# Performance work log

Hardware: AMD Instinct MI355X
Metric: run time of the kernel (lower is better)

Reference implementation:

```python
import jax, jax.numpy as jnp
import numpy as np

N, K, DIM = 50000, 16, 256
SLOPE = 0.2

def _leaky(x):
    return jnp.where(x >= 0, x, SLOPE * x)

def _mlp(x, w, b):
    # torch nn.Linear followed by LeakyReLU(0.2); w is [in, out]
    return _leaky(x @ w + b)

def setup_inputs() -> dict:
    key = jax.random.key(0)
    ks = jax.random.split(key, 14)
    d4, d2 = DIM // 4, DIM // 2
    def lin(k, i, o):
        kw, kb = jax.random.split(k)
        s = 1.0 / np.sqrt(i)
        return (jax.random.uniform(kw, (i, o), jnp.float32, -s, s),
                jax.random.uniform(kb, (o,), jnp.float32, -s, s))
    w_res, b_res = lin(ks[0], DIM, DIM)
    w_init, b_init = lin(ks[1], DIM, d4)
    w_g1, b_g1 = lin(ks[2], 4, d4)
    w_g2, b_g2 = lin(ks[3], 4, d2)
    w_fin, b_fin = lin(ks[4], DIM, DIM)
    return {
        "input_features": jax.random.normal(ks[5], (N, DIM), jnp.float32),
        "geom_features": jax.random.normal(ks[6], (N, K, 4), jnp.float32),
        "closest_indices": jax.random.randint(ks[7], (N, K), 0, N, jnp.int32),
        "w_res": w_res, "b_res": b_res,
        "w_init": w_init, "b_init": b_init,
        "w_g1": w_g1, "b_g1": b_g1,
        "w_g2": w_g2, "b_g2": b_g2,
        "w_fin": w_fin, "b_fin": b_fin,
    }

def _lfa(feat, geom, idx, w_g, b_g):
    # feat: [N, d]; geom: [N, K, 4]; idx: [N, K]
    g = _mlp(geom, w_g, b_g)                 # [N, K, d]
    gathered = feat[idx]                      # [N, K, d] gather over points
    combined = jnp.concatenate([g, gathered], axis=-1)  # [N, K, 2d]
    return jnp.mean(combined, axis=1)         # [N, 2d]

def reference(input_features, geom_features, closest_indices,
              w_res, b_res, w_init, b_init, w_g1, b_g1, w_g2, b_g2,
              w_fin, b_fin):
    residual = _mlp(input_features, w_res, b_res)            # [N, DIM]
    a = _mlp(input_features, w_init, b_init)                 # [N, DIM/4]
    a = _lfa(a, geom_features, closest_indices, w_g1, b_g1)  # [N, DIM/2]
    a = _lfa(a, geom_features, closest_indices, w_g2, b_g2)  # [N, DIM]
    a = _mlp(a, w_fin, b_fin)                                # [N, DIM]
    return a + residual
```

## Files before the change

### kernel.cpp

```cpp
#include <hip/hip_runtime.h>

#define DIM 256
#define KNN 16
#define SLOPE 0.2f

typedef unsigned short u16;
typedef __attribute__((ext_vector_type(8))) unsigned short u16x8;
typedef __attribute__((ext_vector_type(4))) unsigned short u16x4;
typedef __attribute__((ext_vector_type(8))) short s16x8;
typedef __attribute__((ext_vector_type(4))) float f32x4;

__device__ __forceinline__ float leaky(float x) { return x >= 0.f ? x : SLOPE * x; }
__device__ __forceinline__ u16 f2bu(float f) {
    unsigned int u = __float_as_uint(f);
    u = (u + 0x7FFFu + ((u >> 16) & 1u)) >> 16;
    return (u16)u;
}
__device__ __forceinline__ float bu2f(u16 h) {
    return __uint_as_float(((unsigned int)h) << 16);
}

__global__ __launch_bounds__(256) void k_prep(
    const float* __restrict__ w_res, const float* __restrict__ w_init,
    const float* __restrict__ w_fin, u16* __restrict__ wT1, u16* __restrict__ wT3)
{
    const int c = blockIdx.x, t = threadIdx.x;
    if (c < 256)      wT1[c * 256 + t] = f2bu(w_res[t * 256 + c]);
    else if (c < 320) wT1[c * 256 + t] = f2bu(w_init[t * 64 + (c - 256)]);
    else              wT3[(c - 320) * 256 + t] = f2bu(w_fin[t * 256 + (c - 320)]);
}

#define APAD 264
#define BPAD 40
__global__ __launch_bounds__(256) void k_gemm1(
    const float* __restrict__ in, const u16* __restrict__ wT1,
    const float* __restrict__ b_res, const float* __restrict__ b_init,
    float* __restrict__ resid, u16* __restrict__ a1, int N)
{
    __shared__ u16 A_s[64 * APAD];
    __shared__ u16 B_s[320 * BPAD];
    const int t = threadIdx.x;
    const int base = blockIdx.x * 64;

    {
        const int row = t >> 2, seg = t & 3;
        const int grow = min(base + row, N - 1);
        const float* src = in + (size_t)grow * DIM + seg * 64;
        u16* dst = &A_s[row * APAD + seg * 64];
        #pragma unroll
        for (int j = 0; j < 8; ++j) {
            float4 f0 = *(const float4*)(src + j * 8);
            float4 f1 = *(const float4*)(src + j * 8 + 4);
            u16x8 p;
            p[0] = f2bu(f0.x); p[1] = f2bu(f0.y); p[2] = f2bu(f0.z); p[3] = f2bu(f0.w);
            p[4] = f2bu(f1.x); p[5] = f2bu(f1.y); p[6] = f2bu(f1.z); p[7] = f2bu(f1.w);
            *(u16x8*)(dst + j * 8) = p;
        }
    }

    f32x4 acc[4][5];
    #pragma unroll
    for (int i = 0; i < 4; ++i)
        #pragma unroll
        for (int j = 0; j < 5; ++j)
            acc[i][j] = (f32x4){0.f, 0.f, 0.f, 0.f};

    const int w = t >> 6, lane = t & 63;
    const int llow = lane & 15, lhi = lane >> 4;

    for (int ks = 0; ks < 8; ++ks) {
        u16x8 breg[5];
        #pragma unroll
        for (int j = 0; j < 5; ++j) {
            int id = t + 256 * j;
            int col = id >> 2, kg = id & 3;
            breg[j] = *(const u16x8*)(wT1 + col * 256 + ks * 32 + kg * 8);
        }
        __syncthreads();
        #pragma unroll
        for (int j = 0; j < 5; ++j) {
            int id = t + 256 * j;
            int col = id >> 2, kg = id & 3;
            *(u16x8*)(&B_s[col * BPAD + kg * 8]) = breg[j];
        }
        __syncthreads();

        s16x8 afrag[4];
        #pragma unroll
        for (int rt = 0; rt < 4; ++rt)
            afrag[rt] = *(const s16x8*)(&A_s[(rt * 16 + llow) * APAD + ks * 32 + lhi * 8]);
        #pragma unroll
        for (int ci = 0; ci < 5; ++ci) {
            const int ct = w * 5 + ci;
            s16x8 bfrag = *(const s16x8*)(&B_s[(ct * 16 + llow) * BPAD + lhi * 8]);
            #pragma unroll
            for (int rt = 0; rt < 4; ++rt)
                acc[rt][ci] = __builtin_amdgcn_mfma_f32_16x16x32_bf16(
                    afrag[rt], bfrag, acc[rt][ci], 0, 0, 0);
        }
    }

    #pragma unroll
    for (int ci = 0; ci < 5; ++ci) {
        const int ct = w * 5 + ci;
        const int col = ct * 16 + llow;
        if (col < 256) {
            const float bias = b_res[col];
            #pragma unroll
            for (int rt = 0; rt < 4; ++rt)
                #pragma unroll
                for (int r = 0; r < 4; ++r) {
                    int row = base + rt * 16 + lhi * 4 + r;
                    if (row < N)
                        resid[(size_t)row * DIM + col] = leaky(acc[rt][ci][r] + bias);
                }
        } else {
            const int c2 = col - 256;
            const float bias = b_init[c2];
            #pragma unroll
            for (int rt = 0; rt < 4; ++rt)
                #pragma unroll
                for (int r = 0; r < 4; ++r) {
                    int row = base + rt * 16 + lhi * 4 + r;
                    if (row < N)
                        a1[(size_t)row * 64 + c2] = f2bu(leaky(acc[rt][ci][r] + bias));
                }
        }
    }
}

__global__ __launch_bounds__(256) void k_lfa1(
    const float* __restrict__ geom, const int* __restrict__ idx,
    const float* __restrict__ w_g1, const float* __restrict__ b_g1,
    const u16* __restrict__ a1, u16* __restrict__ a2, int N)
{
    __shared__ float geom_s[16 * KNN * 4];
    __shared__ int idx_s[16 * KNN];
    const int t = threadIdx.x;
    const int base = blockIdx.x * 16;

    {
        size_t off = (size_t)base * 64 + t * 4;
        size_t mx = (size_t)N * 64 - 4;
        if (off > mx) off = mx;
        *(float4*)&geom_s[t * 4] = *(const float4*)(geom + off);
        int io = base * KNN + t;
        if (t < 256) idx_s[t] = idx[min(io, N * KNN - 1)];
    }
    __syncthreads();

    const int pt = t >> 4, s = t & 15;
    const int n = base + pt;

    float wr[4][4], bb[4];
    #pragma unroll
    for (int r = 0; r < 4; ++r)
        #pragma unroll
        for (int j = 0; j < 4; ++j)
            wr[r][j] = w_g1[r * 64 + s * 4 + j];
    #pragma unroll
    for (int j = 0; j < 4; ++j) bb[j] = b_g1[s * 4 + j];

    float accM[4] = {0.f, 0.f, 0.f, 0.f};
    const float4* g4 = (const float4*)&geom_s[pt * 64];
    #pragma unroll
    for (int k = 0; k < KNN; ++k) {
        float4 g = g4[k];
        #pragma unroll
        for (int j = 0; j < 4; ++j)
            accM[j] += leaky(g.x * wr[0][j] + g.y * wr[1][j] + g.z * wr[2][j] + g.w * wr[3][j] + bb[j]);
    }

    float accG[4] = {0.f, 0.f, 0.f, 0.f};
    #pragma unroll
    for (int k = 0; k < KNN; ++k) {
        u16x4 u = *(const u16x4*)(a1 + (size_t)idx_s[pt * KNN + k] * 64 + s * 4);
        #pragma unroll
        for (int j = 0; j < 4; ++j) accG[j] += bu2f(u[j]);
    }

    if (n < N) {
        u16x4 pm, pg;
        #pragma unroll
        for (int j = 0; j < 4; ++j) {
            pm[j] = f2bu(accM[j] * 0.0625f);
            pg[j] = f2bu(accG[j] * 0.0625f);
        }
        *(u16x4*)(a2 + (size_t)n * 128 + s * 4) = pm;
        *(u16x4*)(a2 + (size_t)n * 128 + 64 + s * 4) = pg;
    }
}

__global__ __launch_bounds__(256) void k_lfa2_fin(
    const float* __restrict__ geom, const int* __restrict__ idx,
    const float* __restrict__ w_g2, const float* __restrict__ b_g2,
    const u16* __restrict__ a2, const u16* __restrict__ wT3,
    const float* __restrict__ b_fin, float* __restrict__ out, int N)
{
    __shared__ u16 a3_s[64 * APAD];
    __shared__ u16 B_s[256 * BPAD];
    __shared__ float geom_s[64 * KNN * 4];
    __shared__ int idx_s[64 * KNN];
    const int t = threadIdx.x;
    const int base = blockIdx.x * 64;

    {
        size_t mx = (size_t)N * 64 - 4;
        #pragma unroll
        for (int j = 0; j < 4; ++j) {
            size_t off = (size_t)base * 64 + t * 4 + j * 1024;
            if (off > mx) off = mx;
            *(float4*)&geom_s[t * 4 + j * 1024] = *(const float4*)(geom + off);
        }
        int imx = N * KNN - 1;
        #pragma unroll
        for (int j = 0; j < 4; ++j) {
            int off = base * KNN + t + j * 256;
            idx_s[t + j * 256] = idx[min(off, imx)];
        }
    }
    __syncthreads();

    {
        const int c = t & 127, h = t >> 7;
        const float w0 = w_g2[c], w1 = w_g2[128 + c], w2 = w_g2[256 + c],
                    w3 = w_g2[384 + c], bb = b_g2[c];
        for (int p = 0; p < 32; ++p) {
            const int pt = h * 32 + p;
            float acc = 0.f;
            const float4* g4 = (const float4*)&geom_s[pt * 64];
            #pragma unroll
            for (int k = 0; k < KNN; ++k) {
                float4 g = g4[k];
                acc += leaky(g.x * w0 + g.y * w1 + g.z * w2 + g.w * w3 + bb);
            }
            a3_s[pt * APAD + c] = f2bu(acc * 0.0625f);
        }
    }
    {
        const int pt = t >> 2, q = t & 3;
        float acc[32];
        #pragma unroll
        for (int j = 0; j < 32; ++j) acc[j] = 0.f;
        for (int k = 0; k < KNN; ++k) {
            const u16* row = a2 + (size_t)idx_s[pt * KNN + k] * 128 + q * 32;
            #pragma unroll
            for (int v = 0; v < 4; ++v) {
                u16x8 u = *(const u16x8*)(row + v * 8);
                #pragma unroll
                for (int j = 0; j < 8; ++j) acc[v * 8 + j] += bu2f(u[j]);
            }
        }
        #pragma unroll
        for (int v = 0; v < 4; ++v) {
            u16x8 p;
            #pragma unroll
            for (int j = 0; j < 8; ++j) p[j] = f2bu(acc[v * 8 + j] * 0.0625f);
            *(u16x8*)(&a3_s[pt * APAD + 128 + q * 32 + v * 8]) = p;
        }
    }

    f32x4 acc[4][4];
    #pragma unroll
    for (int i = 0; i < 4; ++i)
        #pragma unroll
        for (int j = 0; j < 4; ++j)
            acc[i][j] = (f32x4){0.f, 0.f, 0.f, 0.f};

    const int w = t >> 6, lane = t & 63;
    const int llow = lane & 15, lhi = lane >> 4;

    for (int ks = 0; ks < 8; ++ks) {
        u16x8 breg[4];
        #pragma unroll
        for (int kg = 0; kg < 4; ++kg)
            breg[kg] = *(const u16x8*)(wT3 + t * 256 + ks * 32 + kg * 8);
        __syncthreads();
        #pragma unroll
        for (int kg = 0; kg < 4; ++kg)
            *(u16x8*)(&B_s[t * BPAD + kg * 8]) = breg[kg];
        __syncthreads();

        s16x8 afrag[4];
        #pragma unroll
        for (int rt = 0; rt < 4; ++rt)
            afrag[rt] = *(const s16x8*)(&a3_s[(rt * 16 + llow) * APAD + ks * 32 + lhi * 8]);
        #pragma unroll
        for (int ci = 0; ci < 4; ++ci) {
            const int ct = w * 4 + ci;
            s16x8 bfrag = *(const s16x8*)(&B_s[(ct * 16 + llow) * BPAD + lhi * 8]);
            #pragma unroll
            for (int rt = 0; rt < 4; ++rt)
                acc[rt][ci] = __builtin_amdgcn_mfma_f32_16x16x32_bf16(
                    afrag[rt], bfrag, acc[rt][ci], 0, 0, 0);
        }
    }

    #pragma unroll
    for (int ci = 0; ci < 4; ++ci) {
        const int ct = w * 4 + ci;
        const int col = ct * 16 + llow;
        const float bias = b_fin[col];
        #pragma unroll
        for (int rt = 0; rt < 4; ++rt)
            #pragma unroll
            for (int r = 0; r < 4; ++r) {
                int row = base + rt * 16 + lhi * 4 + r;
                if (row < N) {
                    size_t o = (size_t)row * DIM + col;
                    out[o] = leaky(acc[rt][ci][r] + bias) + out[o];
                }
            }
    }
}

extern "C" void kernel_launch(void* const* d_in, const int* in_sizes, int n_in,
                              void* d_out, int out_size, void* d_ws, size_t ws_size,
                              hipStream_t stream) {
    const float* in    = (const float*)d_in[0];
    const float* geom  = (const float*)d_in[1];
    const int*   idx   = (const int*)d_in[2];
    const float* w_res = (const float*)d_in[3];
    const float* b_res = (const float*)d_in[4];
    const float* w_init= (const float*)d_in[5];
    const float* b_init= (const float*)d_in[6];
    const float* w_g1  = (const float*)d_in[7];
    const float* b_g1  = (const float*)d_in[8];
    const float* w_g2  = (const float*)d_in[9];
    const float* b_g2  = (const float*)d_in[10];
    const float* w_fin = (const float*)d_in[11];
    const float* b_fin = (const float*)d_in[12];
    float* out = (float*)d_out;

    const int N = in_sizes[0] / DIM;

    char* ws = (char*)d_ws;
    u16* a1  = (u16*)ws;
    u16* a2  = (u16*)(ws + (size_t)N * 64 * 2);
    u16* wT1 = (u16*)(ws + (size_t)N * (64 + 128) * 2);
    u16* wT3 = wT1 + 320 * 256;

    k_prep<<<576, 256, 0, stream>>>(w_res, w_init, w_fin, wT1, wT3);
    k_gemm1<<<(N + 63) / 64, 256, 0, stream>>>(in, wT1, b_res, b_init, out, a1, N);
    k_lfa1<<<(N + 15) / 16, 256, 0, stream>>>(geom, idx, w_g1, b_g1, a1, a2, N);
    k_lfa2_fin<<<(N + 63) / 64, 256, 0, stream>>>(geom, idx, w_g2, b_g2, a2, wT3, b_fin, out, N);
}
```

Before: 292.7 us.

## Read GEMM weight fragments directly from global memory, drop LDS staging

Both GEMM kernels now load the B (weight) MFMA fragments straight from global/L2 instead of staging them in shared memory, which removes two barriers per k-step. The fused lfa2 kernel also reads geom and idx directly from global instead of copying them into LDS first. Together these cut LDS usage so more blocks fit per CU, with a launch-bounds hint of 3 blocks, and add unroll pragmas. The cost is that every wave re-reads the weights from cache, and loads are less coalesced, so performance now depends on L2/L1 bandwidth.

```diff
diff --git a/kernel.cpp b/kernel.cpp
--- a/kernel.cpp
+++ b/kernel.cpp
@@ -31,14 +31,12 @@
 }
 
 #define APAD 264
-#define BPAD 40
-__global__ __launch_bounds__(256) void k_gemm1(
+__global__ __launch_bounds__(256, 3) void k_gemm1(
     const float* __restrict__ in, const u16* __restrict__ wT1,
     const float* __restrict__ b_res, const float* __restrict__ b_init,
     float* __restrict__ resid, u16* __restrict__ a1, int N)
 {
     __shared__ u16 A_s[64 * APAD];
-    __shared__ u16 B_s[320 * BPAD];
     const int t = threadIdx.x;
     const int base = blockIdx.x * 64;
 
@@ -57,6 +55,7 @@
             *(u16x8*)(dst + j * 8) = p;
         }
     }
+    __syncthreads();
 
     f32x4 acc[4][5];
     #pragma unroll
@@ -68,23 +67,8 @@
     const int w = t >> 6, lane = t & 63;
     const int llow = lane & 15, lhi = lane >> 4;
 
+    #pragma unroll
     for (int ks = 0; ks < 8; ++ks) {
-        u16x8 breg[5];
-        #pragma unroll
-        for (int j = 0; j < 5; ++j) {
-            int id = t + 256 * j;
-            int col = id >> 2, kg = id & 3;
-            breg[j] = *(const u16x8*)(wT1 + col * 256 + ks * 32 + kg * 8);
-        }
-        __syncthreads();
-        #pragma unroll
-        for (int j = 0; j < 5; ++j) {
-            int id = t + 256 * j;
-            int col = id >> 2, kg = id & 3;
-            *(u16x8*)(&B_s[col * BPAD + kg * 8]) = breg[j];
-        }
-        __syncthreads();
-
         s16x8 afrag[4];
         #pragma unroll
         for (int rt = 0; rt < 4; ++rt)
@@ -92,7 +76,7 @@
         #pragma unroll
         for (int ci = 0; ci < 5; ++ci) {
             const int ct = w * 5 + ci;
-            s16x8 bfrag = *(const s16x8*)(&B_s[(ct * 16 + llow) * BPAD + lhi * 8]);
+            s16x8 bfrag = *(const s16x8*)(wT1 + (size_t)(ct * 16 + llow) * 256 + ks * 32 + lhi * 8);
             #pragma unroll
             for (int rt = 0; rt < 4; ++rt)
                 acc[rt][ci] = __builtin_amdgcn_mfma_f32_16x16x32_bf16(
@@ -145,7 +129,7 @@
         if (off > mx) off = mx;
         *(float4*)&geom_s[t * 4] = *(const float4*)(geom + off);
         int io = base * KNN + t;
-        if (t < 256) idx_s[t] = idx[min(io, N * KNN - 1)];
+        idx_s[t] = idx[min(io, N * KNN - 1)];
     }
     __syncthreads();
 
@@ -191,44 +175,26 @@
     }
 }
 
-__global__ __launch_bounds__(256) void k_lfa2_fin(
+__global__ __launch_bounds__(256, 3) void k_lfa2_fin(
     const float* __restrict__ geom, const int* __restrict__ idx,
     const float* __restrict__ w_g2, const float* __restrict__ b_g2,
     const u16* __restrict__ a2, const u16* __restrict__ wT3,
     const float* __restrict__ b_fin, float* __restrict__ out, int N)
 {
     __shared__ u16 a3_s[64 * APAD];
-    __shared__ u16 B_s[256 * BPAD];
-    __shared__ float geom_s[64 * KNN * 4];
-    __shared__ int idx_s[64 * KNN];
     const int t = threadIdx.x;
     const int base = blockIdx.x * 64;
-
-    {
-        size_t mx = (size_t)N * 64 - 4;
-        #pragma unroll
-        for (int j = 0; j < 4; ++j) {
-            size_t off = (size_t)base * 64 + t * 4 + j * 1024;
-            if (off > mx) off = mx;
-            *(float4*)&geom_s[t * 4 + j * 1024] = *(const float4*)(geom + off);
-        }
-        int imx = N * KNN - 1;
-        #pragma unroll
-        for (int j = 0; j < 4; ++j) {
-            int off = base * KNN + t + j * 256;
-            idx_s[t + j * 256] = idx[min(off, imx)];
-        }
-    }
-    __syncthreads();
 
     {
         const int c = t & 127, h = t >> 7;
         const float w0 = w_g2[c], w1 = w_g2[128 + c], w2 = w_g2[256 + c],
                     w3 = w_g2[384 + c], bb = b_g2[c];
+        #pragma unroll 4
         for (int p = 0; p < 32; ++p) {
             const int pt = h * 32 + p;
+            const int grow = min(base + pt, N - 1);
+            const float4* g4 = (const float4*)(geom + (size_t)grow * 64);
             float acc = 0.f;
-            const float4* g4 = (const float4*)&geom_s[pt * 64];
             #pragma unroll
             for (int k = 0; k < KNN; ++k) {
                 float4 g = g4[k];
@@ -239,11 +205,14 @@
     }
     {
         const int pt = t >> 2, q = t & 3;
+        const int irow = min(base + pt, N - 1);
         float acc[32];
         #pragma unroll
         for (int j = 0; j < 32; ++j) acc[j] = 0.f;
+        #pragma unroll 4
         for (int k = 0; k < KNN; ++k) {
-            const u16* row = a2 + (size_t)idx_s[pt * KNN + k] * 128 + q * 32;
+            const int id = idx[(size_t)irow * KNN + k];
+            const u16* row = a2 + (size_t)id * 128 + q * 32;
             #pragma unroll
             for (int v = 0; v < 4; ++v) {
                 u16x8 u = *(const u16x8*)(row + v * 8);
@@ -259,6 +228,7 @@
             *(u16x8*)(&a3_s[pt * APAD + 128 + q * 32 + v * 8]) = p;
         }
     }
+    __syncthreads();
 
     f32x4 acc[4][4];
     #pragma unroll
@@ -270,17 +240,8 @@
     const int w = t >> 6, lane = t & 63;
     const int llow = lane & 15, lhi = lane >> 4;
 
+    #pragma unroll
     for (int ks = 0; ks < 8; ++ks) {
-        u16x8 breg[4];
-        #pragma unroll
-        for (int kg = 0; kg < 4; ++kg)
-            breg[kg] = *(const u16x8*)(wT3 + t * 256 + ks * 32 + kg * 8);
-        __syncthreads();
-        #pragma unroll
-        for (int kg = 0; kg < 4; ++kg)
-            *(u16x8*)(&B_s[t * BPAD + kg * 8]) = breg[kg];
-        __syncthreads();
-
         s16x8 afrag[4];
         #pragma unroll
         for (int rt = 0; rt < 4; ++rt)
@@ -288,7 +249,7 @@
         #pragma unroll
         for (int ci = 0; ci < 4; ++ci) {
             const int ct = w * 4 + ci;
-            s16x8 bfrag = *(const s16x8*)(&B_s[(ct * 16 + llow) * BPAD + lhi * 8]);
+            s16x8 bfrag = *(const s16x8*)(wT3 + (size_t)(ct * 16 + llow) * 256 + ks * 32 + lhi * 8);
             #pragma unroll
             for (int rt = 0; rt < 4; ++rt)
                 acc[rt][ci] = __builtin_amdgcn_mfma_f32_16x16x32_bf16(
```

Result: slower. 358.4 us (+22.4%).

## Split LFA2 gather into separate high-occupancy kernel before final GEMM

Applied to the files above, without the earlier changes.

The fused lfa2+final-GEMM kernel is split in two. A standalone gather kernel averages neighbour rows of a2 into a half-width buffer a3h, using 16 points per block and all 16 loads issued before any accumulation. The GEMM kernel then loads a3h rows directly into shared memory. lfa1's gather is also batched so all loads are in flight together. This aims to expose more memory-level parallelism for the random gathers, at the cost of an extra launch and a round trip of a3h through global memory. a3h aliases the a1 region, which is assumed dead by then.

```diff
diff --git a/kernel.cpp b/kernel.cpp
--- a/kernel.cpp
+++ b/kernel.cpp
@@ -144,8 +144,7 @@
         size_t mx = (size_t)N * 64 - 4;
         if (off > mx) off = mx;
         *(float4*)&geom_s[t * 4] = *(const float4*)(geom + off);
-        int io = base * KNN + t;
-        if (t < 256) idx_s[t] = idx[min(io, N * KNN - 1)];
+        idx_s[t] = idx[min(base * KNN + t, N * KNN - 1)];
     }
     __syncthreads();
 
@@ -172,12 +171,14 @@
     }
 
     float accG[4] = {0.f, 0.f, 0.f, 0.f};
-    #pragma unroll
-    for (int k = 0; k < KNN; ++k) {
-        u16x4 u = *(const u16x4*)(a1 + (size_t)idx_s[pt * KNN + k] * 64 + s * 4);
-        #pragma unroll
-        for (int j = 0; j < 4; ++j) accG[j] += bu2f(u[j]);
-    }
+    u16x4 v[KNN];
+    #pragma unroll
+    for (int k = 0; k < KNN; ++k)
+        v[k] = *(const u16x4*)(a1 + (size_t)idx_s[pt * KNN + k] * 64 + s * 4);
+    #pragma unroll
+    for (int k = 0; k < KNN; ++k)
+        #pragma unroll
+        for (int j = 0; j < 4; ++j) accG[j] += bu2f(v[k][j]);
 
     if (n < N) {
         u16x4 pm, pg;
@@ -191,16 +192,45 @@
     }
 }
 
-__global__ __launch_bounds__(256) void k_lfa2_fin(
-    const float* __restrict__ geom, const int* __restrict__ idx,
-    const float* __restrict__ w_g2, const float* __restrict__ b_g2,
-    const u16* __restrict__ a2, const u16* __restrict__ wT3,
-    const float* __restrict__ b_fin, float* __restrict__ out, int N)
-{
-    __shared__ u16 a3_s[64 * APAD];
+__global__ __launch_bounds__(256) void k_gather3(
+    const int* __restrict__ idx, const u16* __restrict__ a2,
+    u16* __restrict__ a3h, int N)
+{
+    __shared__ int idx_s[16 * KNN];
+    const int t = threadIdx.x;
+    const int base = blockIdx.x * 16;
+    idx_s[t] = idx[min(base * KNN + t, N * KNN - 1)];
+    __syncthreads();
+
+    const int pt = t >> 4, s = t & 15;
+    const int n = base + pt;
+
+    u16x8 v[KNN];
+    #pragma unroll
+    for (int k = 0; k < KNN; ++k)
+        v[k] = *(const u16x8*)(a2 + (size_t)idx_s[pt * KNN + k] * 128 + s * 8);
+
+    float acc[8] = {0.f, 0.f, 0.f, 0.f, 0.f, 0.f, 0.f, 0.f};
+    #pragma unroll
+    for (int k = 0; k < KNN; ++k)
+        #pragma unroll
+        for (int j = 0; j < 8; ++j) acc[j] += bu2f(v[k][j]);
+
+    u16x8 p;
+    #pragma unroll
+    for (int j = 0; j < 8; ++j) p[j] = f2bu(acc[j] * 0.0625f);
+    if (n < N) *(u16x8*)(a3h + (size_t)n * 128 + s * 8) = p;
+}
+
+__global__ __launch_bounds__(256) void k_gemm3(
+    const float* __restrict__ geom, const float* __restrict__ w_g2,
+    const float* __restrict__ b_g2, const u16* __restrict__ a3h,
+    const u16* __restrict__ wT3, const float* __restrict__ b_fin,
+    float* __restrict__ out, int N)
+{
+    __shared__ u16 A_s[64 * APAD];
     __shared__ u16 B_s[256 * BPAD];
-    __shared__ float geom_s[64 * KNN * 4];
-    __shared__ int idx_s[64 * KNN];
+    __shared__ float geom_s[64 * 64];
     const int t = threadIdx.x;
     const int base = blockIdx.x * 64;
 
@@ -212,12 +242,13 @@
             if (off > mx) off = mx;
             *(float4*)&geom_s[t * 4 + j * 1024] = *(const float4*)(geom + off);
         }
-        int imx = N * KNN - 1;
-        #pragma unroll
-        for (int j = 0; j < 4; ++j) {
-            int off = base * KNN + t + j * 256;
-            idx_s[t + j * 256] = idx[min(off, imx)];
-        }
+        const int row = t >> 2, q = t & 3;
+        const int grow = min(base + row, N - 1);
+        const u16* src = a3h + (size_t)grow * 128 + q * 32;
+        u16* dst = &A_s[row * APAD + 128 + q * 32];
+        #pragma unroll
+        for (int j = 0; j < 4; ++j)
+            *(u16x8*)(dst + j * 8) = *(const u16x8*)(src + j * 8);
     }
     __syncthreads();
 
@@ -225,38 +256,17 @@
         const int c = t & 127, h = t >> 7;
         const float w0 = w_g2[c], w1 = w_g2[128 + c], w2 = w_g2[256 + c],
                     w3 = w_g2[384 + c], bb = b_g2[c];
+        #pragma unroll 4
         for (int p = 0; p < 32; ++p) {
             const int pt = h * 32 + p;
+            const float4* g4 = (const float4*)&geom_s[pt * 64];
             float acc = 0.f;
-            const float4* g4 = (const float4*)&geom_s[pt * 64];
             #pragma unroll
             for (int k = 0; k < KNN; ++k) {
                 float4 g = g4[k];
                 acc += leaky(g.x * w0 + g.y * w1 + g.z * w2 + g.w * w3 + bb);
             }
-            a3_s[pt * APAD + c] = f2bu(acc * 0.0625f);
-        }
-    }
-    {
-        const int pt = t >> 2, q = t & 3;
-        float acc[32];
-        #pragma unroll
-        for (int j = 0; j < 32; ++j) acc[j] = 0.f;
-        for (int k = 0; k < KNN; ++k) {
-            const u16* row = a2 + (size_t)idx_s[pt * KNN + k] * 128 + q * 32;
-            #pragma unroll
-            for (int v = 0; v < 4; ++v) {
-                u16x8 u = *(const u16x8*)(row + v * 8);
-                #pragma unroll
-                for (int j = 0; j < 8; ++j) acc[v * 8 + j] += bu2f(u[j]);
-            }
-        }
-        #pragma unroll
-        for (int v = 0; v < 4; ++v) {
-            u16x8 p;
-            #pragma unroll
-            for (int j = 0; j < 8; ++j) p[j] = f2bu(acc[v * 8 + j] * 0.0625f);
-            *(u16x8*)(&a3_s[pt * APAD + 128 + q * 32 + v * 8]) = p;
+            A_s[pt * APAD + c] = f2bu(acc * 0.0625f);
         }
     }
 
@@ -284,7 +294,7 @@
         s16x8 afrag[4];
         #pragma unroll
         for (int rt = 0; rt < 4; ++rt)
-            afrag[rt] = *(const s16x8*)(&a3_s[(rt * 16 + llow) * APAD + ks * 32 + lhi * 8]);
+            afrag[rt] = *(const s16x8*)(&A_s[(rt * 16 + llow) * APAD + ks * 32 + lhi * 8]);
         #pragma unroll
         for (int ci = 0; ci < 4; ++ci) {
             const int ct = w * 4 + ci;
@@ -336,12 +346,14 @@
 
     char* ws = (char*)d_ws;
     u16* a1  = (u16*)ws;
-    u16* a2  = (u16*)(ws + (size_t)N * 64 * 2);
-    u16* wT1 = (u16*)(ws + (size_t)N * (64 + 128) * 2);
+    u16* a3h = (u16*)ws;
+    u16* a2  = (u16*)(ws + (size_t)N * 128 * 2);
+    u16* wT1 = (u16*)(ws + (size_t)N * 256 * 2);
     u16* wT3 = wT1 + 320 * 256;
 
     k_prep<<<576, 256, 0, stream>>>(w_res, w_init, w_fin, wT1, wT3);
     k_gemm1<<<(N + 63) / 64, 256, 0, stream>>>(in, wT1, b_res, b_init, out, a1, N);
     k_lfa1<<<(N + 15) / 16, 256, 0, stream>>>(geom, idx, w_g1, b_g1, a1, a2, N);
-    k_lfa2_fin<<<(N + 63) / 64, 256, 0, stream>>>(geom, idx, w_g2, b_g2, a2, wT3, b_fin, out, N);
-}
+    k_gather3<<<(N + 15) / 16, 256, 0, stream>>>(idx, a2, a3h, N);
+    k_gemm3<<<(N + 63) / 64, 256, 0, stream>>>(geom, w_g2, b_g2, a3h, wT3, b_fin, out, N);
+}
```

Measured after the change: 310.3 us. 1.06x slower.
